# Optimization experiments

Measured on AMD Instinct MI355X. Metric: run time of the kernel, lower is better.

Reference implementation:

```python
import jax, jax.numpy as jnp
import numpy as np

N = 100_000   # nodes
E = 1_600_000 # edges
F = 16        # input node features
H = 32        # embedding_size
B = 256       # graphs in batch


def setup_inputs() -> dict:
    key = jax.random.key(0)
    ks = jax.random.split(key, 13)
    s = 0.1  # small init scale for weights
    return {
        "x": jax.random.normal(ks[0], (N, F), jnp.float32),
        "edge_index": jax.random.randint(ks[1], (2, E), 0, N, dtype=jnp.int64),
        "batch_index": jnp.sort(jax.random.randint(ks[2], (N,), 0, B, dtype=jnp.int64)),
        "W0": jax.random.normal(ks[3], (F, H), jnp.float32) * s,
        "b0": jax.random.normal(ks[4], (H,), jnp.float32) * s,
        "W1": jax.random.normal(ks[5], (H, H), jnp.float32) * s,
        "b1": jax.random.normal(ks[6], (H,), jnp.float32) * s,
        "W2": jax.random.normal(ks[7], (H, H), jnp.float32) * s,
        "b2": jax.random.normal(ks[8], (H,), jnp.float32) * s,
        "W3": jax.random.normal(ks[9], (H, H), jnp.float32) * s,
        "b3": jax.random.normal(ks[10], (H, H), jnp.float32)[:, 0] * s,
        "W_out": jax.random.normal(ks[11], (3 * H, 1), jnp.float32) * s,
        "b_out": jax.random.normal(ks[12], (1,), jnp.float32) * s,
    }


def _gcn_forward(x, edge_index, batch_index,
                 W0, b0, W1, b1, W2, b2, W3, b3, W_out, b_out):
    src, dst = edge_index[0], edge_index[1]
    n = x.shape[0]
    # GCN symmetric normalization with self-loops: deg includes the +1 self-loop
    deg = jax.ops.segment_sum(jnp.ones(src.shape[0], x.dtype), dst, num_segments=n) + 1.0
    dinv = jax.lax.rsqrt(deg)
    edge_coef = (dinv[src] * dinv[dst])[:, None]   # [E,1]
    self_coef = (dinv * dinv)[:, None]             # [N,1]

    def conv(h, W, b):
        # x' = D^{-1/2}(A+I)D^{-1/2} (h W) + b  (PyG GCNConv)
        hW = h @ W
        agg = jax.ops.segment_sum(hW[src] * edge_coef, dst, num_segments=n)
        agg = agg + hW * self_coef  # self-loop contribution
        return agg + b

    h = jnp.tanh(conv(x, W0, b0))
    h = jnp.tanh(conv(h, W1, b1))
    h = jnp.tanh(conv(h, W2, b2))
    h = jnp.tanh(conv(h, W3, b3))

    # Global max / mean / add pooling over batch_index
    gmax = jax.ops.segment_max(h, batch_index, num_segments=B)
    gsum = jax.ops.segment_sum(h, batch_index, num_segments=B)
    cnt = jax.ops.segment_sum(jnp.ones(n, h.dtype), batch_index, num_segments=B)
    gmean = gsum / jnp.maximum(cnt, 1.0)[:, None]
    pooled = jnp.concatenate([gmax, gmean, gsum], axis=1)  # [B, 3H]

    out = pooled @ W_out + b_out  # [B, 1]
    return out, pooled


def reference(x, edge_index, batch_index,
              W0, b0, W1, b1, W2, b2, W3, b3, W_out, b_out):
    return _gcn_forward(x, edge_index, batch_index,
                        W0, b0, W1, b1, W2, b2, W3, b3, W_out, b_out)
```

## Files before the change

kernel.cpp:

```cpp
#include <hip/hip_runtime.h>
#include <math.h>

#define N_NODES 100000
#define N_EDGES 1600000
#define F_IN    16
#define H_DIM   32
#define B_GRAPHS 256

#define BSHIFT  7
#define BSIZE   128
#define NBUCKET ((N_NODES + BSIZE - 1) / BSIZE)
#define EPB     8192
#define NCHUNK  ((N_EDGES + EPB - 1) / EPB)
#define CAPB    2560
#define CSTRIDE 2944
#define TPAD    (NBUCKET * CSTRIDE)
#define CURSTR  16
#define NPB     16
#define LAYER_BLOCKS (N_NODES / NPB)

typedef int   v4i __attribute__((ext_vector_type(4)));
typedef float v2f __attribute__((ext_vector_type(2)));

#if defined(__has_builtin)
#if __has_builtin(__builtin_amdgcn_cvt_pk_f32_fp8) && __has_builtin(__builtin_amdgcn_cvt_pk_fp8_f32)
#define HW_FP8 1
#endif
#endif

__device__ inline float bf_lo(unsigned u) { return __uint_as_float(u << 16); }
__device__ inline float bf_hi(unsigned u) { return __uint_as_float(u & 0xffff0000u); }
__device__ inline unsigned pack_bf16x2(float a, float b) {
    unsigned ua = __float_as_uint(a), ub = __float_as_uint(b);
    ua += 0x7fffu + ((ua >> 16) & 1u);
    ub += 0x7fffu + ((ub >> 16) & 1u);
    return (ua >> 16) | (ub & 0xffff0000u);
}

__device__ inline unsigned sw_f32_to_fp8(float v) {
    unsigned u = __float_as_uint(v * 0x1.0p-120f);
    unsigned s = (u >> 24) & 0x80u;
    u &= 0x7FFFFFFFu;
    u += 0x7FFFFu + ((u >> 20) & 1u);
    unsigned em = u >> 20;
    if (em > 0x7Eu) em = 0x7Eu;
    return s | em;
}
__device__ inline float sw_fp8_to_f32(unsigned b) {
    unsigned s  = (b & 0x80u) << 24;
    unsigned em = (b & 0x7Fu) << 20;
    return __uint_as_float(s | em) * 0x1.0p120f;
}

__device__ inline v2f fp8x2_to_f32x2(unsigned u) {
#ifdef HW_FP8
    return __builtin_amdgcn_cvt_pk_f32_fp8(u & 0xFFFFu, false);
#else
    v2f r; r.x = sw_fp8_to_f32(u & 0xFF); r.y = sw_fp8_to_f32((u >> 8) & 0xFF); return r;
#endif
}
__device__ inline unsigned short f32x2_to_fp8x2(float a, float b) {
#ifdef HW_FP8
    return (unsigned short)__builtin_amdgcn_cvt_pk_fp8_f32(a, b, 0, false);
#else
    return (unsigned short)(sw_f32_to_fp8(a) | (sw_f32_to_fp8(b) << 8));
#endif
}

__global__ __launch_bounds__(256) void init_cur_kernel(int* __restrict__ bucket_cur) {
    int b = blockIdx.x * 256 + threadIdx.x;
    if (b < NBUCKET) bucket_cur[b * CURSTR] = b * CAPB;
}

__global__ __launch_bounds__(1024) void passB_kernel(const int* __restrict__ ei,
                                                     int* __restrict__ bucket_cur,
                                                     unsigned* __restrict__ rec_out) {
    __shared__ int hist[NBUCKET];
    __shared__ int gcur[NBUCKET];
    int t = threadIdx.x;
    for (int k = t; k < NBUCKET; k += 1024) hist[k] = 0;
    __syncthreads();

    const int* dst = ei + N_EDGES;
    int base = blockIdx.x * EPB;
    int end  = base + EPB; if (end > N_EDGES) end = N_EDGES;

    for (int e = base + t; e < end; e += 1024) atomicAdd(&hist[dst[e] >> BSHIFT], 1);
    __syncthreads();

    for (int k = t; k < NBUCKET; k += 1024) {
        int h = hist[k];
        gcur[k] = h ? atomicAdd(&bucket_cur[k * CURSTR], h) : 0;
    }
    __syncthreads();

    for (int e = base + t; e < end; e += 1024) {
        int d = dst[e], s = ei[e];
        int bk = d >> BSHIFT;
        int pos = atomicAdd(&gcur[bk], 1);
        rec_out[pos] = (unsigned)s | ((unsigned)(d & (BSIZE - 1)) << 20);
    }
}

__global__ __launch_bounds__(256) void dinv_kernel(const unsigned* __restrict__ rec,
                                                   const int* __restrict__ bucket_cur,
                                                   float* __restrict__ dinv) {
    __shared__ int cnt[BSIZE];
    int t = threadIdx.x, b = blockIdx.x;
    if (t < BSIZE) cnt[t] = 0;
    __syncthreads();
    int e1 = bucket_cur[b * CURSTR];
    for (int e = b * CAPB + t; e < e1; e += 256) atomicAdd(&cnt[rec[e] >> 20], 1);
    __syncthreads();
    int nd = (b << BSHIFT) + t;
    if (t < BSIZE && nd < N_NODES) dinv[nd] = rsqrtf((float)cnt[t] + 1.0f);
}

__global__ __launch_bounds__(256) void passC_kernel(const unsigned* __restrict__ rec,
                                                    const int* __restrict__ bucket_cur,
                                                    const float* __restrict__ dinv,
                                                    int2* __restrict__ row_meta,
                                                    int2* __restrict__ csr) {
    __shared__ unsigned stage[CAPB];
    __shared__ int cnt[BSIZE];
    __shared__ int pds[BSIZE];
    __shared__ int cur[BSIZE];
    __shared__ float sdv[BSIZE];
    int t = threadIdx.x, b = blockIdx.x;
    int node0 = b << BSHIFT;
    int e0 = b * CAPB;
    int n = bucket_cur[b * CURSTR] - e0;
    int pbase = b * CSTRIDE;
    if (t < BSIZE) {
        cnt[t] = 0;
        int nd = node0 + t;
        sdv[t] = (nd < N_NODES) ? dinv[nd] : 0.f;
    }
    __syncthreads();
    for (int k = t; k < n; k += 256) {
        unsigned r = rec[e0 + k];
        stage[k] = r;
        atomicAdd(&cnt[r >> 20], 1);
    }
    __syncthreads();
    int pd = 0;
    if (t < BSIZE) { pd = (cnt[t] + 3) & ~3; pds[t] = pd; }
    __syncthreads();
    for (int off = 1; off < BSIZE; off <<= 1) {
        int v = (t < BSIZE && t >= off) ? pds[t - off] : 0;
        __syncthreads();
        if (t < BSIZE) pds[t] += v;
        __syncthreads();
    }
    if (t < BSIZE) {
        int startp = pbase + pds[t] - pd;
        cur[t] = startp;
        int nd = node0 + t;
        if (nd < N_NODES) {
            row_meta[nd] = make_int2(startp, pd);
            for (int k = startp + cnt[t]; k < startp + pd; ++k)
                csr[k] = make_int2(nd, 0);
        }
    }
    __syncthreads();
    for (int k = t; k < n; k += 256) {
        unsigned r = stage[k];
        int dl = r >> 20;
        int s  = r & 0xFFFFF;
        int pos = atomicAdd(&cur[dl], 1);
        csr[pos] = make_int2(s, __float_as_int(dinv[s] * sdv[dl]));
    }
}

template <int FIN, bool PACKED>
__global__ __launch_bounds__(256) void layer_kernel(
        const void* __restrict__ h_in_v,
        const int2* __restrict__ row_meta,
        const v4i* __restrict__ csr4,
        const float* __restrict__ dinv,
        const float* __restrict__ W,
        const float* __restrict__ bias,
        unsigned short* __restrict__ out8,
        unsigned* __restrict__ outbf) {
    constexpr int STR = FIN + 1;
    __shared__ float sW[FIN * H_DIM];
    __shared__ float sb[H_DIM];
    __shared__ float agg[NPB][STR];
    int t = threadIdx.x;
    for (int k = t; k < FIN * H_DIM; k += 256) sW[k] = W[k];
    if (t < H_DIM) sb[t] = bias[t];

    int nl = t >> 4, ln = t & 15;
    int i = blockIdx.x * NPB + nl;
    int2 m = row_meta[i];
    float di = dinv[i], di2 = di * di;
    int q    = m.x >> 1;
    int qend = (m.x + m.y) >> 1;

    if (PACKED) {
        const unsigned short* hp = (const unsigned short*)h_in_v;
        v2f sf = fp8x2_to_f32x2(hp[i * 16 + ln]);
        float acc0 = sf.x * di2, acc1 = sf.y * di2;
        for (; q + 8 <= qend; q += 8) {
            v4i ca[8];
#pragma unroll
            for (int k = 0; k < 8; ++k) ca[k] = __builtin_nontemporal_load(&csr4[q + k]);
            unsigned v[16];
#pragma unroll
            for (int k = 0; k < 8; ++k) {
                v[2 * k]     = hp[ca[k].x * 16 + ln];
                v[2 * k + 1] = hp[ca[k].z * 16 + ln];
            }
#pragma unroll
            for (int k = 0; k < 8; ++k) {
                float c0 = __int_as_float(ca[k].y), c1 = __int_as_float(ca[k].w);
                v2f f0 = fp8x2_to_f32x2(v[2 * k]);
                v2f f1 = fp8x2_to_f32x2(v[2 * k + 1]);
                acc0 += f0.x * c0 + f1.x * c1;
                acc1 += f0.y * c0 + f1.y * c1;
            }
        }
        if (q + 4 <= qend) {
            v4i ca[4];
#pragma unroll
            for (int k = 0; k < 4; ++k) ca[k] = __builtin_nontemporal_load(&csr4[q + k]);
#pragma unroll
            for (int k = 0; k < 4; ++k) {
                v2f f0 = fp8x2_to_f32x2(hp[ca[k].x * 16 + ln]);
                v2f f1 = fp8x2_to_f32x2(hp[ca[k].z * 16 + ln]);
                float c0 = __int_as_float(ca[k].y), c1 = __int_as_float(ca[k].w);
                acc0 += f0.x * c0 + f1.x * c1;
                acc1 += f0.y * c0 + f1.y * c1;
            }
            q += 4;
        }
        if (q < qend) {
            v4i a = __builtin_nontemporal_load(&csr4[q]);
            v4i b = __builtin_nontemporal_load(&csr4[q + 1]);
            v2f f0 = fp8x2_to_f32x2(hp[a.x * 16 + ln]);
            v2f f1 = fp8x2_to_f32x2(hp[a.z * 16 + ln]);
            v2f f2 = fp8x2_to_f32x2(hp[b.x * 16 + ln]);
            v2f f3 = fp8x2_to_f32x2(hp[b.z * 16 + ln]);
            float c0 = __int_as_float(a.y), c1 = __int_as_float(a.w);
            float c2 = __int_as_float(b.y), c3 = __int_as_float(b.w);
            acc0 += f0.x * c0 + f1.x * c1 + f2.x * c2 + f3.x * c3;
            acc1 += f0.y * c0 + f1.y * c1 + f2.y * c2 + f3.y * c3;
        }
        agg[nl][2 * ln]     = acc0;
        agg[nl][2 * ln + 1] = acc1;
    } else {
        const float* xf = (const float*)h_in_v;
        float acc = xf[i * F_IN + ln] * di2;
        for (; q + 8 <= qend; q += 8) {
            v4i ca[8];
#pragma unroll
            for (int k = 0; k < 8; ++k) ca[k] = __builtin_nontemporal_load(&csr4[q + k]);
            float v[16];
#pragma unroll
            for (int k = 0; k < 8; ++k) {
                v[2 * k]     = xf[ca[k].x * F_IN + ln];
                v[2 * k + 1] = xf[ca[k].z * F_IN + ln];
            }
#pragma unroll
            for (int k = 0; k < 8; ++k)
                acc += v[2 * k] * __int_as_float(ca[k].y)
                     + v[2 * k + 1] * __int_as_float(ca[k].w);
        }
        if (q + 4 <= qend) {
            v4i ca[4];
#pragma unroll
            for (int k = 0; k < 4; ++k) ca[k] = __builtin_nontemporal_load(&csr4[q + k]);
#pragma unroll
            for (int k = 0; k < 4; ++k)
                acc += xf[ca[k].x * F_IN + ln] * __int_as_float(ca[k].y)
                     + xf[ca[k].z * F_IN + ln] * __int_as_float(ca[k].w);
            q += 4;
        }
        if (q < qend) {
            v4i a = __builtin_nontemporal_load(&csr4[q]);
            v4i b = __builtin_nontemporal_load(&csr4[q + 1]);
            acc += xf[a.x * F_IN + ln] * __int_as_float(a.y)
                 + xf[a.z * F_IN + ln] * __int_as_float(a.w)
                 + xf[b.x * F_IN + ln] * __int_as_float(b.y)
                 + xf[b.z * F_IN + ln] * __int_as_float(b.w);
        }
        agg[nl][ln] = acc;
    }
    __syncthreads();

    int j0 = 2 * ln;
    float o0 = sb[j0], o1 = sb[j0 + 1];
    const float* arow = &agg[nl][0];
#pragma unroll
    for (int k = 0; k < FIN; ++k) {
        float a = arow[k];
        o0 += a * sW[k * H_DIM + j0];
        o1 += a * sW[k * H_DIM + j0 + 1];
    }
    o0 = tanhf(o0); o1 = tanhf(o1);
    if (out8)  out8[i * 16 + ln]  = f32x2_to_fp8x2(o0, o1);
    if (outbf) outbf[i * 16 + ln] = pack_bf16x2(o0, o1);
}

__global__ __launch_bounds__(256) void pool_kernel(const unsigned* __restrict__ hp,
                                                   const int* __restrict__ batch,
                                                   const float* __restrict__ Wout,
                                                   const float* __restrict__ bout,
                                                   float* __restrict__ out) {
    int b = blockIdx.x;
    int t = threadIdx.x;
    int lane_n = t >> 5;
    int j = t & 31;

    int lo = 0, hi = N_NODES;
    while (lo < hi) { int mid = (lo + hi) >> 1; if (batch[mid] < b) lo = mid + 1; else hi = mid; }
    int start = lo;
    hi = N_NODES;
    while (lo < hi) { int mid = (lo + hi) >> 1; if (batch[mid] < b + 1) lo = mid + 1; else hi = mid; }
    int end = lo;

    float vmax = -INFINITY, vsum = 0.f;
    for (int i = start + lane_n; i < end; i += 8) {
        unsigned q = hp[i * 16 + (j >> 1)];
        float v = (j & 1) ? bf_hi(q) : bf_lo(q);
        vmax = fmaxf(vmax, v);
        vsum += v;
    }

    __shared__ float smax[8][32];
    __shared__ float ssum[8][32];
    __shared__ float pool96[96];
    smax[lane_n][j] = vmax;
    ssum[lane_n][j] = vsum;
    __syncthreads();

    if (t < 32) {
        float m = smax[0][t], s = ssum[0][t];
#pragma unroll
        for (int n = 1; n < 8; ++n) { m = fmaxf(m, smax[n][t]); s += ssum[n][t]; }
        int cnt = end - start;
        float mean = s / fmaxf((float)cnt, 1.0f);
        pool96[t]      = m;
        pool96[32 + t] = mean;
        pool96[64 + t] = s;
    }
    __syncthreads();

    if (t < 96) out[B_GRAPHS + b * 96 + t] = pool96[t];

    __shared__ float dotbuf[96];
    if (t < 96) dotbuf[t] = pool96[t] * Wout[t];
    __syncthreads();
    if (t == 0) {
        float acc = 0.f;
#pragma unroll
        for (int k = 0; k < 96; ++k) acc += dotbuf[k];
        out[b] = acc + bout[0];
    }
}

extern "C" void kernel_launch(void* const* d_in, const int* in_sizes, int n_in,
                              void* d_out, int out_size, void* d_ws, size_t ws_size,
                              hipStream_t stream) {
    const float* x     = (const float*)d_in[0];
    const int*   ei    = (const int*)  d_in[1];
    const int*   batch = (const int*)  d_in[2];
    const float* W0    = (const float*)d_in[3];
    const float* b0    = (const float*)d_in[4];
    const float* W1    = (const float*)d_in[5];
    const float* b1    = (const float*)d_in[6];
    const float* W2    = (const float*)d_in[7];
    const float* b2    = (const float*)d_in[8];
    const float* W3    = (const float*)d_in[9];
    const float* b3    = (const float*)d_in[10];
    const float* Wout  = (const float*)d_in[11];
    const float* bout  = (const float*)d_in[12];
    float* out = (float*)d_out;

    char* p = (char*)d_ws;
    float*          dinv       = (float*)p;          p += (size_t)N_NODES * 4;
    unsigned short* h8A        = (unsigned short*)p; p += (size_t)N_NODES * 16 * 2;
    unsigned short* h8B        = (unsigned short*)p; p += (size_t)N_NODES * 16 * 2;
    unsigned*       rec        = (unsigned*)p;       p += (size_t)NBUCKET * CAPB * 4;
    int2*           csr        = (int2*)p;           p += (size_t)TPAD * 8;
    int2*           row_meta   = (int2*)p;           p += (size_t)N_NODES * 8;
    int*            bucket_cur = (int*)p;            p += (size_t)NBUCKET * CURSTR * 4;
    unsigned* hBF = rec;

    init_cur_kernel<<<(NBUCKET + 255) / 256, 256, 0, stream>>>(bucket_cur);
    passB_kernel<<<NCHUNK, 1024, 0, stream>>>(ei, bucket_cur, rec);
    dinv_kernel<<<NBUCKET, 256, 0, stream>>>(rec, bucket_cur, dinv);
    passC_kernel<<<NBUCKET, 256, 0, stream>>>(rec, bucket_cur, dinv, row_meta, csr);

    layer_kernel<F_IN, false><<<LAYER_BLOCKS, 256, 0, stream>>>(
        x,   row_meta, (const v4i*)csr, dinv, W0, b0, h8A, (unsigned*)nullptr);
    layer_kernel<H_DIM, true><<<LAYER_BLOCKS, 256, 0, stream>>>(
        h8A, row_meta, (const v4i*)csr, dinv, W1, b1, h8B, (unsigned*)nullptr);
    layer_kernel<H_DIM, true><<<LAYER_BLOCKS, 256, 0, stream>>>(
        h8B, row_meta, (const v4i*)csr, dinv, W2, b2, h8A, (unsigned*)nullptr);
    layer_kernel<H_DIM, true><<<LAYER_BLOCKS, 256, 0, stream>>>(
        h8A, row_meta, (const v4i*)csr, dinv, W3, b3, (unsigned short*)nullptr, hBF);

    pool_kernel<<<B_GRAPHS, 256, 0, stream>>>(hBF, batch, Wout, bout, out);
}
```

Measured before the change: 307.9 us.

## Pad CSR rows to 16 and restructure hidden layers with 8-lane shuffled edge loads

Each CSR row is now padded to a multiple of 16 edges, with a larger per-bucket stride to fit the extra padding. Layers 0 and 1-3 get separate kernels. The hidden-layer kernel handles 32 nodes per block with 8 lanes per node. Each lane loads 4 fp8 features as one 32-bit word, and the lanes load one CSR vector each and share the edge indices and coefficients via shuffles. This is meant to remove redundant per-lane CSR loads and tail branches and to raise the bytes fetched per gather, at the cost of more padding edges and a larger CSR buffer.

```diff
diff --git a/kernel.cpp b/kernel.cpp
--- a/kernel.cpp
+++ b/kernel.cpp
@@ -13,11 +13,13 @@
 #define EPB     8192
 #define NCHUNK  ((N_EDGES + EPB - 1) / EPB)
 #define CAPB    2560
-#define CSTRIDE 2944
+#define CSTRIDE 3584
 #define TPAD    (NBUCKET * CSTRIDE)
 #define CURSTR  16
-#define NPB     16
-#define LAYER_BLOCKS (N_NODES / NPB)
+#define NPB0    16
+#define L0_BLOCKS (N_NODES / NPB0)
+#define NPB8    32
+#define L8_BLOCKS (N_NODES / NPB8)
 
 typedef int   v4i __attribute__((ext_vector_type(4)));
 typedef float v2f __attribute__((ext_vector_type(2)));
@@ -28,14 +30,14 @@
 #endif
 #endif
 
-__device__ inline float bf_lo(unsigned u) { return __uint_as_float(u << 16); }
-__device__ inline float bf_hi(unsigned u) { return __uint_as_float(u & 0xffff0000u); }
 __device__ inline unsigned pack_bf16x2(float a, float b) {
     unsigned ua = __float_as_uint(a), ub = __float_as_uint(b);
     ua += 0x7fffu + ((ua >> 16) & 1u);
     ub += 0x7fffu + ((ub >> 16) & 1u);
     return (ua >> 16) | (ub & 0xffff0000u);
 }
+__device__ inline float bf_lo(unsigned u) { return __uint_as_float(u << 16); }
+__device__ inline float bf_hi(unsigned u) { return __uint_as_float(u & 0xffff0000u); }
 
 __device__ inline unsigned sw_f32_to_fp8(float v) {
     unsigned u = __float_as_uint(v * 0x1.0p-120f);
@@ -51,12 +53,13 @@
     unsigned em = (b & 0x7Fu) << 20;
     return __uint_as_float(s | em) * 0x1.0p120f;
 }
-
-__device__ inline v2f fp8x2_to_f32x2(unsigned u) {
+template <bool HI>
+__device__ inline v2f fp8pk(unsigned u) {
 #ifdef HW_FP8
-    return __builtin_amdgcn_cvt_pk_f32_fp8(u & 0xFFFFu, false);
+    return __builtin_amdgcn_cvt_pk_f32_fp8((int)u, HI);
 #else
-    v2f r; r.x = sw_fp8_to_f32(u & 0xFF); r.y = sw_fp8_to_f32((u >> 8) & 0xFF); return r;
+    unsigned h = HI ? (u >> 16) : (u & 0xFFFFu);
+    v2f r; r.x = sw_fp8_to_f32(h & 0xFF); r.y = sw_fp8_to_f32((h >> 8) & 0xFF); return r;
 #endif
 }
 __device__ inline unsigned short f32x2_to_fp8x2(float a, float b) {
@@ -144,7 +147,7 @@
     }
     __syncthreads();
     int pd = 0;
-    if (t < BSIZE) { pd = (cnt[t] + 3) & ~3; pds[t] = pd; }
+    if (t < BSIZE) { pd = (cnt[t] + 15) & ~15; pds[t] = pd; }
     __syncthreads();
     for (int off = 1; off < BSIZE; off <<= 1) {
         int v = (t < BSIZE && t >= off) ? pds[t - off] : 0;
@@ -172,134 +175,128 @@
     }
 }
 
-template <int FIN, bool PACKED>
-__global__ __launch_bounds__(256) void layer_kernel(
-        const void* __restrict__ h_in_v,
+__global__ __launch_bounds__(256) void layer0_kernel(
+        const float* __restrict__ xf,
         const int2* __restrict__ row_meta,
         const v4i* __restrict__ csr4,
         const float* __restrict__ dinv,
         const float* __restrict__ W,
         const float* __restrict__ bias,
-        unsigned short* __restrict__ out8,
-        unsigned* __restrict__ outbf) {
-    constexpr int STR = FIN + 1;
-    __shared__ float sW[FIN * H_DIM];
+        unsigned short* __restrict__ out8) {
+    __shared__ float sW[F_IN * H_DIM];
     __shared__ float sb[H_DIM];
-    __shared__ float agg[NPB][STR];
+    __shared__ float agg[NPB0][F_IN + 1];
     int t = threadIdx.x;
-    for (int k = t; k < FIN * H_DIM; k += 256) sW[k] = W[k];
+    for (int k = t; k < F_IN * H_DIM; k += 256) sW[k] = W[k];
     if (t < H_DIM) sb[t] = bias[t];
 
     int nl = t >> 4, ln = t & 15;
-    int i = blockIdx.x * NPB + nl;
+    int i = blockIdx.x * NPB0 + nl;
     int2 m = row_meta[i];
     float di = dinv[i], di2 = di * di;
     int q    = m.x >> 1;
     int qend = (m.x + m.y) >> 1;
 
-    if (PACKED) {
-        const unsigned short* hp = (const unsigned short*)h_in_v;
-        v2f sf = fp8x2_to_f32x2(hp[i * 16 + ln]);
-        float acc0 = sf.x * di2, acc1 = sf.y * di2;
-        for (; q + 8 <= qend; q += 8) {
-            v4i ca[8];
-#pragma unroll
-            for (int k = 0; k < 8; ++k) ca[k] = __builtin_nontemporal_load(&csr4[q + k]);
-            unsigned v[16];
-#pragma unroll
-            for (int k = 0; k < 8; ++k) {
-                v[2 * k]     = hp[ca[k].x * 16 + ln];
-                v[2 * k + 1] = hp[ca[k].z * 16 + ln];
-            }
-#pragma unroll
-            for (int k = 0; k < 8; ++k) {
-                float c0 = __int_as_float(ca[k].y), c1 = __int_as_float(ca[k].w);
-                v2f f0 = fp8x2_to_f32x2(v[2 * k]);
-                v2f f1 = fp8x2_to_f32x2(v[2 * k + 1]);
-                acc0 += f0.x * c0 + f1.x * c1;
-                acc1 += f0.y * c0 + f1.y * c1;
-            }
+    float acc = xf[i * F_IN + ln] * di2;
+    for (; q + 8 <= qend; q += 8) {
+        v4i ca[8];
+#pragma unroll
+        for (int k = 0; k < 8; ++k) ca[k] = __builtin_nontemporal_load(&csr4[q + k]);
+        float v[16];
+#pragma unroll
+        for (int k = 0; k < 8; ++k) {
+            v[2 * k]     = xf[ca[k].x * F_IN + ln];
+            v[2 * k + 1] = xf[ca[k].z * F_IN + ln];
         }
-        if (q + 4 <= qend) {
-            v4i ca[4];
-#pragma unroll
-            for (int k = 0; k < 4; ++k) ca[k] = __builtin_nontemporal_load(&csr4[q + k]);
-#pragma unroll
-            for (int k = 0; k < 4; ++k) {
-                v2f f0 = fp8x2_to_f32x2(hp[ca[k].x * 16 + ln]);
-                v2f f1 = fp8x2_to_f32x2(hp[ca[k].z * 16 + ln]);
-                float c0 = __int_as_float(ca[k].y), c1 = __int_as_float(ca[k].w);
-                acc0 += f0.x * c0 + f1.x * c1;
-                acc1 += f0.y * c0 + f1.y * c1;
-            }
-            q += 4;
-        }
-        if (q < qend) {
-            v4i a = __builtin_nontemporal_load(&csr4[q]);
-            v4i b = __builtin_nontemporal_load(&csr4[q + 1]);
-            v2f f0 = fp8x2_to_f32x2(hp[a.x * 16 + ln]);
-            v2f f1 = fp8x2_to_f32x2(hp[a.z * 16 + ln]);
-            v2f f2 = fp8x2_to_f32x2(hp[b.x * 16 + ln]);
-            v2f f3 = fp8x2_to_f32x2(hp[b.z * 16 + ln]);
-            float c0 = __int_as_float(a.y), c1 = __int_as_float(a.w);
-            float c2 = __int_as_float(b.y), c3 = __int_as_float(b.w);
-            acc0 += f0.x * c0 + f1.x * c1 + f2.x * c2 + f3.x * c3;
-            acc1 += f0.y * c0 + f1.y * c1 + f2.y * c2 + f3.y * c3;
-        }
-        agg[nl][2 * ln]     = acc0;
-        agg[nl][2 * ln + 1] = acc1;
-    } else {
-        const float* xf = (const float*)h_in_v;
-        float acc = xf[i * F_IN + ln] * di2;
-        for (; q + 8 <= qend; q += 8) {
-            v4i ca[8];
-#pragma unroll
-            for (int k = 0; k < 8; ++k) ca[k] = __builtin_nontemporal_load(&csr4[q + k]);
-            float v[16];
-#pragma unroll
-            for (int k = 0; k < 8; ++k) {
-                v[2 * k]     = xf[ca[k].x * F_IN + ln];
-                v[2 * k + 1] = xf[ca[k].z * F_IN + ln];
-            }
-#pragma unroll
-            for (int k = 0; k < 8; ++k)
-                acc += v[2 * k] * __int_as_float(ca[k].y)
-                     + v[2 * k + 1] * __int_as_float(ca[k].w);
-        }
-        if (q + 4 <= qend) {
-            v4i ca[4];
-#pragma unroll
-            for (int k = 0; k < 4; ++k) ca[k] = __builtin_nontemporal_load(&csr4[q + k]);
-#pragma unroll
-            for (int k = 0; k < 4; ++k)
-                acc += xf[ca[k].x * F_IN + ln] * __int_as_float(ca[k].y)
-                     + xf[ca[k].z * F_IN + ln] * __int_as_float(ca[k].w);
-            q += 4;
-        }
-        if (q < qend) {
-            v4i a = __builtin_nontemporal_load(&csr4[q]);
-            v4i b = __builtin_nontemporal_load(&csr4[q + 1]);
-            acc += xf[a.x * F_IN + ln] * __int_as_float(a.y)
-                 + xf[a.z * F_IN + ln] * __int_as_float(a.w)
-                 + xf[b.x * F_IN + ln] * __int_as_float(b.y)
-                 + xf[b.z * F_IN + ln] * __int_as_float(b.w);
-        }
-        agg[nl][ln] = acc;
-    }
+#pragma unroll
+        for (int k = 0; k < 8; ++k)
+            acc += v[2 * k] * __int_as_float(ca[k].y)
+                 + v[2 * k + 1] * __int_as_float(ca[k].w);
+    }
+    agg[nl][ln] = acc;
     __syncthreads();
 
     int j0 = 2 * ln;
     float o0 = sb[j0], o1 = sb[j0 + 1];
     const float* arow = &agg[nl][0];
 #pragma unroll
-    for (int k = 0; k < FIN; ++k) {
+    for (int k = 0; k < F_IN; ++k) {
         float a = arow[k];
         o0 += a * sW[k * H_DIM + j0];
         o1 += a * sW[k * H_DIM + j0 + 1];
     }
-    o0 = tanhf(o0); o1 = tanhf(o1);
-    if (out8)  out8[i * 16 + ln]  = f32x2_to_fp8x2(o0, o1);
-    if (outbf) outbf[i * 16 + ln] = pack_bf16x2(o0, o1);
+    out8[i * 16 + ln] = f32x2_to_fp8x2(tanhf(o0), tanhf(o1));
+}
+
+template <bool FINAL>
+__global__ __launch_bounds__(256) void layer8_kernel(
+        const unsigned* __restrict__ hp32,
+        const int2* __restrict__ row_meta,
+        const v4i* __restrict__ csr4,
+        const float* __restrict__ dinv,
+        const float* __restrict__ W,
+        const float* __restrict__ bias,
+        unsigned* __restrict__ out32,
+        unsigned* __restrict__ outbf) {
+    __shared__ float sW[H_DIM * H_DIM];
+    __shared__ float sb[H_DIM];
+    __shared__ float agg[NPB8][H_DIM + 1];
+    int t = threadIdx.x;
+    for (int k = t; k < H_DIM * H_DIM; k += 256) sW[k] = W[k];
+    if (t < H_DIM) sb[t] = bias[t];
+
+    int nl = t >> 3, ln = t & 7;
+    int i = blockIdx.x * NPB8 + nl;
+    int2 m = row_meta[i];
+    float di = dinv[i], di2 = di * di;
+
+    unsigned su = hp32[i * 8 + ln];
+    v2f slo = fp8pk<false>(su), shi = fp8pk<true>(su);
+    float a0 = slo.x * di2, a1 = slo.y * di2, a2 = shi.x * di2, a3 = shi.y * di2;
+
+    int q4 = m.x >> 1;
+    int nch = m.y >> 4;
+    for (int c = 0; c < nch; ++c) {
+        v4i ca = __builtin_nontemporal_load(&csr4[q4 + c * 8 + ln]);
+        unsigned v[16]; float cf[16];
+#pragma unroll
+        for (int k = 0; k < 16; ++k) {
+            int sk = __shfl((k & 1) ? ca.z : ca.x, k >> 1, 8);
+            cf[k]  = __int_as_float(__shfl((k & 1) ? ca.w : ca.y, k >> 1, 8));
+            v[k] = hp32[sk * 8 + ln];
+        }
+#pragma unroll
+        for (int k = 0; k < 16; ++k) {
+            v2f lo = fp8pk<false>(v[k]), hi = fp8pk<true>(v[k]);
+            a0 += lo.x * cf[k]; a1 += lo.y * cf[k];
+            a2 += hi.x * cf[k]; a3 += hi.y * cf[k];
+        }
+    }
+    agg[nl][4 * ln]     = a0;
+    agg[nl][4 * ln + 1] = a1;
+    agg[nl][4 * ln + 2] = a2;
+    agg[nl][4 * ln + 3] = a3;
+    __syncthreads();
+
+    int j0 = 4 * ln;
+    float o0 = sb[j0], o1 = sb[j0 + 1], o2 = sb[j0 + 2], o3 = sb[j0 + 3];
+    const float* arow = &agg[nl][0];
+#pragma unroll
+    for (int k = 0; k < H_DIM; ++k) {
+        float a = arow[k];
+        o0 += a * sW[k * H_DIM + j0];
+        o1 += a * sW[k * H_DIM + j0 + 1];
+        o2 += a * sW[k * H_DIM + j0 + 2];
+        o3 += a * sW[k * H_DIM + j0 + 3];
+    }
+    o0 = tanhf(o0); o1 = tanhf(o1); o2 = tanhf(o2); o3 = tanhf(o3);
+    if (!FINAL) {
+        out32[i * 8 + ln] = (unsigned)f32x2_to_fp8x2(o0, o1)
+                          | ((unsigned)f32x2_to_fp8x2(o2, o3) << 16);
+    } else {
+        outbf[i * 16 + 2 * ln]     = pack_bf16x2(o0, o1);
+        outbf[i * 16 + 2 * ln + 1] = pack_bf16x2(o2, o3);
+    }
 }
 
 __global__ __launch_bounds__(256) void pool_kernel(const unsigned* __restrict__ hp,
@@ -392,14 +389,17 @@
     dinv_kernel<<<NBUCKET, 256, 0, stream>>>(rec, bucket_cur, dinv);
     passC_kernel<<<NBUCKET, 256, 0, stream>>>(rec, bucket_cur, dinv, row_meta, csr);
 
-    layer_kernel<F_IN, false><<<LAYER_BLOCKS, 256, 0, stream>>>(
-        x,   row_meta, (const v4i*)csr, dinv, W0, b0, h8A, (unsigned*)nullptr);
-    layer_kernel<H_DIM, true><<<LAYER_BLOCKS, 256, 0, stream>>>(
-        h8A, row_meta, (const v4i*)csr, dinv, W1, b1, h8B, (unsigned*)nullptr);
-    layer_kernel<H_DIM, true><<<LAYER_BLOCKS, 256, 0, stream>>>(
-        h8B, row_meta, (const v4i*)csr, dinv, W2, b2, h8A, (unsigned*)nullptr);
-    layer_kernel<H_DIM, true><<<LAYER_BLOCKS, 256, 0, stream>>>(
-        h8A, row_meta, (const v4i*)csr, dinv, W3, b3, (unsigned short*)nullptr, hBF);
+    layer0_kernel<<<L0_BLOCKS, 256, 0, stream>>>(
+        x, row_meta, (const v4i*)csr, dinv, W0, b0, h8A);
+    layer8_kernel<false><<<L8_BLOCKS, 256, 0, stream>>>(
+        (const unsigned*)h8A, row_meta, (const v4i*)csr, dinv, W1, b1,
+        (unsigned*)h8B, (unsigned*)nullptr);
+    layer8_kernel<false><<<L8_BLOCKS, 256, 0, stream>>>(
+        (const unsigned*)h8B, row_meta, (const v4i*)csr, dinv, W2, b2,
+        (unsigned*)h8A, (unsigned*)nullptr);
+    layer8_kernel<true><<<L8_BLOCKS, 256, 0, stream>>>(
+        (const unsigned*)h8A, row_meta, (const v4i*)csr, dinv, W3, b3,
+        (unsigned*)nullptr, hBF);
 
     pool_kernel<<<B_GRAPHS, 256, 0, stream>>>(hBF, batch, Wout, bout, out);
 }
```

After: 283.1 us. 8.1% less time.
